# Performance work log

Measured on AMD Instinct MI355X. Metric: run time of the kernel, lower is better.

Reference implementation:

```python
import jax, jax.numpy as jnp
import numpy as np

FEATURE_DIM = 256
LN_EPS = 1e-5        # torch nn.LayerNorm default
WHITEN_EPS = 1e-4    # whitening_eps init arg


def setup_inputs() -> dict:
    key = jax.random.key(0)
    k1, _ = jax.random.split(key)
    B, T, D = 64, 2048, FEATURE_DIM
    x = jax.random.normal(k1, (B, T, D), dtype=jnp.float32)
    gamma = jnp.ones((D,), dtype=jnp.float32)
    beta = jnp.zeros((D,), dtype=jnp.float32)
    return {"x": x, "gamma": gamma, "beta": beta}


def reference(x, gamma, beta):
    # x: (B, T, D)
    B, T, D = x.shape
    # LayerNorm over last dim
    mean = jnp.mean(x, axis=-1, keepdims=True)
    var = jnp.mean((x - mean) ** 2, axis=-1, keepdims=True)
    xn = (x - mean) * jax.lax.rsqrt(var + LN_EPS) * gamma + beta
    # Batched cross-frame covariance whitening (T >= 2 here)
    mu = jnp.mean(xn, axis=1, keepdims=True)          # (B, 1, D)
    xc = xn - mu                                       # (B, T, D)
    cov = jnp.einsum('btd,bte->bde', xc, xc) / (T - 1) # (B, D, D)
    cov = cov + WHITEN_EPS * jnp.eye(D, dtype=x.dtype)
    eigvals, eigvecs = jnp.linalg.eigh(cov)            # (B, D), (B, D, D)
    inv_sqrt_vals = jax.lax.rsqrt(jnp.clip(eigvals, WHITEN_EPS, None))  # (B, D)
    # inv_sqrt = V diag(w^-1/2) V^T
    inv_sqrt = jnp.einsum('bde,be,bfe->bdf', eigvecs, inv_sqrt_vals, eigvecs)
    out = jnp.einsum('btd,bdf->btf', xc, inv_sqrt)
    return out
```

## Files before the change

kernel.cpp:

```cpp
#include <hip/hip_runtime.h>
#include <cstddef>

#define TT 2048
#define BB 64
#define DD 256
#define LN_EPS 1e-5f
#define WEPS 1e-4f

typedef __attribute__((ext_vector_type(8))) short short8;
typedef __attribute__((ext_vector_type(4))) float f32x4;
typedef __attribute__((ext_vector_type(8))) _Float16 f16x8;
typedef __attribute__((ext_vector_type(4))) _Float16 f16x4;

__device__ __forceinline__ unsigned short f2h(float f) {
  _Float16 h = (_Float16)f;
  return *(unsigned short*)&h;
}
__device__ __forceinline__ float h2f(unsigned short u) {
  _Float16 h = *(_Float16*)&u;
  return (float)h;
}
__device__ __forceinline__ void gload16(unsigned short* lds, const unsigned short* g) {
  __builtin_amdgcn_global_load_lds(
      (const __attribute__((address_space(1))) void*)g,
      (__attribute__((address_space(3))) void*)lds, 16, 0, 0);
}

__global__ __launch_bounds__(256) void prepass_kernel(const float* __restrict__ x,
    const float* __restrict__ gamma, const float* __restrict__ beta,
    unsigned short* __restrict__ A, float* __restrict__ part) {
  int c = blockIdx.x;
  int b = blockIdx.y;
  int tid = threadIdx.x;
  int wave = tid >> 6, lane = tid & 63;
  int rowbase = b * TT + c * 128 + wave * 32;
  const float* xb = x + (size_t)rowbase * DD + lane * 4;
  unsigned short* Ab = A + (size_t)rowbase * DD + lane * 4;
  float4 g4 = *(const float4*)&gamma[lane * 4];
  float4 b4 = *(const float4*)&beta[lane * 4];
  float a0 = 0.f, a1 = 0.f, a2 = 0.f, a3 = 0.f;
  for (int i = 0; i < 32; ++i) {
    float4 v = *(const float4*)&xb[(size_t)i * DD];
    float s  = v.x + v.y + v.z + v.w;
    float sq = v.x*v.x + v.y*v.y + v.z*v.z + v.w*v.w;
    #pragma unroll
    for (int off = 32; off; off >>= 1) { s += __shfl_xor(s, off); sq += __shfl_xor(sq, off); }
    float mean = s * (1.f/DD);
    float var  = fmaxf(sq * (1.f/DD) - mean*mean, 0.f);
    float rstd = rsqrtf(var + LN_EPS);
    float c0 = (v.x - mean) * rstd, c1 = (v.y - mean) * rstd;
    float c2 = (v.z - mean) * rstd, c3 = (v.w - mean) * rstd;
    a0 += c0; a1 += c1; a2 += c2; a3 += c3;
    ushort4 w;
    w.x = f2h(c0 * g4.x + b4.x);
    w.y = f2h(c1 * g4.y + b4.y);
    w.z = f2h(c2 * g4.z + b4.z);
    w.w = f2h(c3 * g4.w + b4.w);
    *(ushort4*)&Ab[(size_t)i * DD] = w;
  }
  int pidx = c * 4 + wave;
  *(float4*)&part[((size_t)pidx*BB + b)*DD + lane*4] = make_float4(a0, a1, a2, a3);
}

__global__ __launch_bounds__(256) void mu_finalize_kernel(const float* __restrict__ part,
                                                          const float* __restrict__ gamma,
                                                          const float* __restrict__ beta,
                                                          float* __restrict__ mu) {
  int b = blockIdx.x;
  int d = threadIdx.x;
  float s = 0.f;
  #pragma unroll 8
  for (int c = 0; c < 64; ++c) s += part[((size_t)c*BB + b)*DD + d];
  mu[b*DD + d] = gamma[d] * s * (1.f/TT) + beta[d];
}

__global__ __launch_bounds__(256) void cov_mfma(const unsigned short* __restrict__ A,
    const float* __restrict__ mu, unsigned short* __restrict__ Ch) {
  int flat = blockIdx.y * gridDim.x + blockIdx.x;
  int kx = flat & 7, j = flat >> 3;
  int b = (kx << 3) + j / 10;
  int tile = j - (j / 10) * 10;
  int p = 0, t = tile;
  while (t >= 4 - p) { t -= (4 - p); ++p; }
  int q = p + t;
  int i0 = p * 64, j0 = q * 64;
  bool diag = (p == q);

  __shared__ unsigned short sm[16384];
  __shared__ float sMu[128];

  int tid = threadIdx.x;
  const float* mub = mu + (size_t)b*DD;
  if (tid < 64) { sMu[tid] = mub[i0+tid]; sMu[64+tid] = mub[j0+tid]; }
  __syncthreads();

  int wave = tid >> 6, lane = tid & 63;
  int lr = lane & 15, lg = lane >> 4;
  int tg4 = tid >> 4;
  int dg  = tid & 15;
  int d0 = dg * 4;
  const unsigned short* Ab = A + (size_t)b*TT*DD;

  int ch16 = tg4 >> 1, half = tg4 & 1;
  int widx[4];
  #pragma unroll
  for (int jj = 0; jj < 4; ++jj) {
    int dl = d0 + jj;
    int swz = (ch16 ^ (dl & 7) ^ ((dl >> 3) & 7)) & 7;
    widx[jj] = dl*64 + swz*8 + half*4;
  }

  f32x4 acc[4] = {};

  #define COV_STAGE(k0v, dst)                                                  \
  {                                                                            \
    int trow = (k0v) + tg4 * 4;                                                \
    ushort4 sv0 = *(const ushort4*)&Ab[(size_t)(trow+0)*DD + i0 + d0];         \
    ushort4 sv1 = *(const ushort4*)&Ab[(size_t)(trow+1)*DD + i0 + d0];         \
    ushort4 sv2 = *(const ushort4*)&Ab[(size_t)(trow+2)*DD + i0 + d0];         \
    ushort4 sv3 = *(const ushort4*)&Ab[(size_t)(trow+3)*DD + i0 + d0];         \
    { ushort4 w = {sv0.x, sv1.x, sv2.x, sv3.x}; *(ushort4*)&(dst)[widx[0]] = w; } \
    { ushort4 w = {sv0.y, sv1.y, sv2.y, sv3.y}; *(ushort4*)&(dst)[widx[1]] = w; } \
    { ushort4 w = {sv0.z, sv1.z, sv2.z, sv3.z}; *(ushort4*)&(dst)[widx[2]] = w; } \
    { ushort4 w = {sv0.w, sv1.w, sv2.w, sv3.w}; *(ushort4*)&(dst)[widx[3]] = w; } \
    if (!diag) {                                                               \
      ushort4 t0v = *(const ushort4*)&Ab[(size_t)(trow+0)*DD + j0 + d0];       \
      ushort4 t1v = *(const ushort4*)&Ab[(size_t)(trow+1)*DD + j0 + d0];       \
      ushort4 t2v = *(const ushort4*)&Ab[(size_t)(trow+2)*DD + j0 + d0];       \
      ushort4 t3v = *(const ushort4*)&Ab[(size_t)(trow+3)*DD + j0 + d0];       \
      { ushort4 w = {t0v.x, t1v.x, t2v.x, t3v.x}; *(ushort4*)&(dst)[4096 + widx[0]] = w; } \
      { ushort4 w = {t0v.y, t1v.y, t2v.y, t3v.y}; *(ushort4*)&(dst)[4096 + widx[1]] = w; } \
      { ushort4 w = {t0v.z, t1v.z, t2v.z, t3v.z}; *(ushort4*)&(dst)[4096 + widx[2]] = w; } \
      { ushort4 w = {t0v.w, t1v.w, t2v.w, t3v.w}; *(ushort4*)&(dst)[4096 + widx[3]] = w; } \
    }                                                                          \
  }

  COV_STAGE(0, sm);
  __syncthreads();

  for (int kk = 0; kk < 32; ++kk) {
    unsigned short* cur = sm + (kk & 1) * 8192;
    if (kk < 31) {
      unsigned short* nxt = sm + ((kk & 1) ^ 1) * 8192;
      COV_STAGE((kk + 1) * 64, nxt);
    }
    const unsigned short* pA = cur;
    const unsigned short* pB = diag ? cur : (cur + 4096);
    #pragma unroll
    for (int ks = 0; ks < 2; ++ks) {
      int rowA = wave*16 + lr;
      int cc = ks*4 + lg;
      int aoff = rowA*64 + (((cc ^ (rowA&7) ^ ((rowA>>3)&7)) & 7) << 3);
      f16x8 av = *(const f16x8*)&pA[aoff];
      #pragma unroll
      for (int n = 0; n < 4; ++n) {
        int rowB = n*16 + lr;
        int boff = rowB*64 + (((cc ^ (rowB&7) ^ ((rowB>>3)&7)) & 7) << 3);
        f16x8 bv = *(const f16x8*)&pB[boff];
        acc[n] = __builtin_amdgcn_mfma_f32_16x16x32_f16(av, bv, acc[n], 0, 0, 0);
      }
    }
    __syncthreads();
  }
  #undef COV_STAGE

  float* sC = (float*)sm;
  #pragma unroll
  for (int n = 0; n < 4; ++n)
    #pragma unroll
    for (int r = 0; r < 4; ++r)
      sC[(wave*16 + lg*4 + r)*65 + n*16 + lr] = acc[n][r];
  __syncthreads();
  unsigned short* Chb = Ch + (size_t)b*DD*DD;
  const float invTm1 = 1.f / (float)(TT - 1);
  int row = tid >> 2, cb = (tid & 3) * 16;
  int gi = i0 + row;
  float mi = sMu[row] * (float)TT;
  unsigned short hv[16];
  #pragma unroll
  for (int e = 0; e < 16; ++e) {
    int gj = j0 + cb + e;
    float v = (sC[row*65 + cb + e] - mi * sMu[64 + cb + e]) * invTm1;
    if (gi == gj) v += WEPS;
    hv[e] = f2h(v);
    if (!diag) Chb[(size_t)gj*DD + gi] = hv[e];
  }
  size_t go = (size_t)gi*DD + j0 + cb;
  *(short8*)&Chb[go]     = *(short8*)&hv[0];
  *(short8*)&Chb[go + 8] = *(short8*)&hv[8];
}

__global__ __launch_bounds__(256) void power_kernel(
    const unsigned short* __restrict__ Ch, float* __restrict__ sbuf) {
  int b = blockIdx.x, tid = threadIdx.x;
  __shared__ unsigned short sC[DD*DD];
  __shared__ float v[DD];
  __shared__ float red[4];
  const unsigned short* Cb = Ch + (size_t)b*DD*DD;
  #pragma unroll
  for (int i = 0; i < 32; ++i) {
    int chunkid = i*256 + tid;
    int r = chunkid >> 5, ch = chunkid & 31;
    short8 qv = *(const short8*)&Cb[(size_t)chunkid*8];
    *(short8*)&sC[r*256 + ((ch ^ (r & 7)) << 3)] = qv;
  }
  unsigned u = (unsigned)tid * 2654435761u;
  v[tid] = 0.5f + (float)((u >> 9) & 1023) * (1.f/1024.f);
  __syncthreads();
  float lam = 1.f;
  for (int it = 0; it < 10; ++it) {
    float w = 0.f;
    #pragma unroll
    for (int ch = 0; ch < 32; ++ch) {
      short8 hq = *(const short8*)&sC[tid*256 + ((ch ^ (tid & 7)) << 3)];
      const float* vp = &v[ch*8];
      #pragma unroll
      for (int e = 0; e < 8; ++e) w += h2f((unsigned short)hq[e]) * vp[e];
    }
    float ssq = w * w;
    #pragma unroll
    for (int off = 32; off; off >>= 1) ssq += __shfl_xor(ssq, off);
    if ((tid & 63) == 0) red[tid >> 6] = ssq;
    __syncthreads();
    float nrm = sqrtf(red[0] + red[1] + red[2] + red[3]);
    lam = nrm;
    v[tid] = w / nrm;
    __syncthreads();
  }
  if (tid == 0) sbuf[b] = lam * 1.05f;
}

__device__ __forceinline__ void bgemm_tile2(
    const unsigned short* __restrict__ A, const unsigned short* __restrict__ B,
    unsigned short* __restrict__ C,
    float alpha, float diagBeta, int tilex, int b, unsigned short* sm) {
  const int tid = threadIdx.x;
  const int i0g = (tilex >> 1) * 128, j0g = (tilex & 1) * 128;
  const size_t mb = (size_t)b * DD * DD;
  const int wave = tid >> 6, lane = tid & 63;
  const int wr = wave >> 2, wc = wave & 3;
  const int lr = lane & 15, lg = lane >> 4;

  f32x4 acc[8] = {};

  #pragma unroll
  for (int p2 = 0; p2 < 2; ++p2) {
    int slot = tid + p2 * 512;
    int row = slot >> 3, c = slot & 7;
    int srcc = (c ^ (row & 7)) << 3;
    int base = (wave * 64 + p2 * 512) * 8;
    gload16(&sm[base], A + mb + (size_t)(i0g + row) * DD + srcc);
    gload16(&sm[8192 + base], B + mb + (size_t)(j0g + row) * DD + srcc);
  }
  __syncthreads();

  #pragma unroll
  for (int kk = 0; kk < 4; ++kk) {
    unsigned short* cur = sm + (kk & 1) * 16384;
    if (kk < 3) {
      unsigned short* nxt = sm + ((kk & 1) ^ 1) * 16384;
      int k0n = (kk + 1) * 64;
      #pragma unroll
      for (int p2 = 0; p2 < 2; ++p2) {
        int slot = tid + p2 * 512;
        int row = slot >> 3, c = slot & 7;
        int srcc = (c ^ (row & 7)) << 3;
        int base = (wave * 64 + p2 * 512) * 8;
        gload16(&nxt[base], A + mb + (size_t)(i0g + row) * DD + k0n + srcc);
        gload16(&nxt[8192 + base], B + mb + (size_t)(j0g + row) * DD + k0n + srcc);
      }
    }
    #pragma unroll
    for (int ks = 0; ks < 2; ++ks) {
      int cc = ks * 4 + lg;
      f16x8 bv[2];
      #pragma unroll
      for (int n = 0; n < 2; ++n) {
        int rowB = wc * 32 + n * 16 + lr;
        int boff = rowB * 64 + ((cc ^ (rowB & 7)) * 8);
        bv[n] = *(const f16x8*)&cur[8192 + boff];
      }
      #pragma unroll
      for (int m = 0; m < 4; ++m) {
        int rowA = wr * 64 + m * 16 + lr;
        int aoff = rowA * 64 + ((cc ^ (rowA & 7)) * 8);
        f16x8 av = *(const f16x8*)&cur[aoff];
        #pragma unroll
        for (int n = 0; n < 2; ++n)
          acc[m*2+n] = __builtin_amdgcn_mfma_f32_16x16x32_f16(av, bv[n], acc[m*2+n], 0, 0, 0);
      }
    }
    __syncthreads();
  }

  #pragma unroll
  for (int m = 0; m < 4; ++m) {
    #pragma unroll
    for (int n = 0; n < 2; ++n) {
      int col = j0g + wc * 32 + n * 16 + lr;
      int row0 = i0g + wr * 64 + m * 16 + lg * 4;
      #pragma unroll
      for (int r = 0; r < 4; ++r) {
        float vv = alpha * acc[m*2+n][r];
        int row = row0 + r;
        if (row == col) vv += diagBeta;
        C[mb + (size_t)row * DD + col] = f2h(vv);
      }
    }
  }
}

__global__ __launch_bounds__(512) void bgemm_mfma2(
    const unsigned short* __restrict__ A, const unsigned short* __restrict__ B,
    unsigned short* __restrict__ C, float alpha, float diagBeta) {
  __shared__ unsigned short sm[32768];
  int flat = blockIdx.y * gridDim.x + blockIdx.x;
  int kx = flat & 7, j = flat >> 3;
  int b = (kx << 3) + (j >> 2);
  int tile = j & 3;
  bgemm_tile2(A, B, C, alpha, diagBeta, tile, b, sm);
}

__global__ __launch_bounds__(512) void bgemm_dual2(
    const unsigned short* __restrict__ A0, const unsigned short* __restrict__ B0,
    unsigned short* __restrict__ C0,
    const unsigned short* __restrict__ A1, const unsigned short* __restrict__ B1,
    unsigned short* __restrict__ C1) {
  __shared__ unsigned short sm[32768];
  int flat = blockIdx.y * gridDim.x + blockIdx.x;
  int kx = flat & 7, j = flat >> 3;
  int b = (kx << 3) + (j >> 3);
  int t8 = j & 7;
  int half = t8 >> 2, tile = t8 & 3;
  if (half == 0)
    bgemm_tile2(A0, B0, C0, 0.5f, 0.f, tile, b, sm);
  else
    bgemm_tile2(A1, B1, C1, 0.5f, 0.f, tile, b, sm);
}

__global__ __launch_bounds__(512) void bgemm_p0(
    const unsigned short* __restrict__ C, unsigned short* __restrict__ Y1,
    unsigned short* __restrict__ Z1, const float* __restrict__ sbuf) {
  __shared__ unsigned short sm[32768];
  int flat = blockIdx.y * gridDim.x + blockIdx.x;
  int kx = flat & 7, j = flat >> 3;
  int b = (kx << 3) + (j >> 2);
  int tilex = j & 3;

  const int tid = threadIdx.x;
  const int i0g = (tilex >> 1) * 128, j0g = (tilex & 1) * 128;
  const size_t mb = (size_t)b * DD * DD;
  const int wave = tid >> 6, lane = tid & 63;
  const int wr = wave >> 2, wc = wave & 3;
  const int lr = lane & 15, lg = lane >> 4;

  f32x4 acc[8] = {};

  #pragma unroll
  for (int p2 = 0; p2 < 2; ++p2) {
    int slot = tid + p2 * 512;
    int row = slot >> 3, c = slot & 7;
    int srcc = (c ^ (row & 7)) << 3;
    int base = (wave * 64 + p2 * 512) * 8;
    gload16(&sm[base], C + mb + (size_t)(i0g + row) * DD + srcc);
    gload16(&sm[8192 + base], C + mb + (size_t)(j0g + row) * DD + srcc);
  }
  __syncthreads();

  #pragma unroll
  for (int kk = 0; kk < 4; ++kk) {
    unsigned short* cur = sm + (kk & 1) * 16384;
    if (kk < 3) {
      unsigned short* nxt = sm + ((kk & 1) ^ 1) * 16384;
      int k0n = (kk + 1) * 64;
      #pragma unroll
      for (int p2 = 0; p2 < 2; ++p2) {
        int slot = tid + p2 * 512;
        int row = slot >> 3, c = slot & 7;
        int srcc = (c ^ (row & 7)) << 3;
        int base = (wave * 64 + p2 * 512) * 8;
        gload16(&nxt[base], C + mb + (size_t)(i0g + row) * DD + k0n + srcc);
        gload16(&nxt[8192 + base], C + mb + (size_t)(j0g + row) * DD + k0n + srcc);
      }
    }
    #pragma unroll
    for (int ks = 0; ks < 2; ++ks) {
      int cc = ks * 4 + lg;
      f16x8 bv[2];
      #pragma unroll
      for (int n = 0; n < 2; ++n) {
        int rowB = wc * 32 + n * 16 + lr;
        int boff = rowB * 64 + ((cc ^ (rowB & 7)) * 8);
        bv[n] = *(const f16x8*)&cur[8192 + boff];
      }
      #pragma unroll
      for (int m = 0; m < 4; ++m) {
        int rowA = wr * 64 + m * 16 + lr;
        int aoff = rowA * 64 + ((cc ^ (rowA & 7)) * 8);
        f16x8 av = *(const f16x8*)&cur[aoff];
        #pragma unroll
        for (int n = 0; n < 2; ++n)
          acc[m*2+n] = __builtin_amdgcn_mfma_f32_16x16x32_f16(av, bv[n], acc[m*2+n], 0, 0, 0);
      }
    }
    __syncthreads();
  }

  float invs = 1.f / sbuf[b];
  float a2 = -invs * invs;
  float a1c = 2.f * invs;
  float z1c = -invs;
  #pragma unroll
  for (int m = 0; m < 4; ++m) {
    #pragma unroll
    for (int n = 0; n < 2; ++n) {
      int col = j0g + wc * 32 + n * 16 + lr;
      int row0 = i0g + wr * 64 + m * 16 + lg * 4;
      #pragma unroll
      for (int r = 0; r < 4; ++r) {
        int row = row0 + r;
        float cv = h2f(C[mb + (size_t)row * DD + col]);
        float yv = a2 * acc[m*2+n][r] + a1c * cv;
        float zv = z1c * cv + ((row == col) ? 2.f : 0.f);
        Y1[mb + (size_t)row * DD + col] = f2h(yv);
        Z1[mb + (size_t)row * DD + col] = f2h(zv);
      }
    }
  }
}

__global__ __launch_bounds__(256) void matvec_r(const float* __restrict__ mu,
    const unsigned short* __restrict__ W, float* __restrict__ rvec) {
  int b = blockIdx.x, f = threadIdx.x;
  __shared__ float sMu[DD];
  sMu[f] = mu[(size_t)b*DD + f];
  __syncthreads();
  const unsigned short* Wb = W + (size_t)b*DD*DD;
  float acc = 0.f;
  #pragma unroll 8
  for (int d = 0; d < DD; ++d) acc += sMu[d] * h2f(Wb[(size_t)d*DD + f]);
  rvec[(size_t)b*DD + f] = acc;
}

__global__ __launch_bounds__(512) void out_mfma2(const unsigned short* __restrict__ A,
    const unsigned short* __restrict__ W, const float* __restrict__ rvec,
    const float* __restrict__ sbuf, float* __restrict__ out) {
  int flat = blockIdx.y * gridDim.x + blockIdx.x;
  int kx = flat & 7, j = flat >> 3;
  int b = (kx << 3) + (j >> 5);
  int tile = j & 31;
  int t0 = (tile >> 1) * 128, f0 = (tile & 1) * 128;
  __shared__ unsigned short sm[32768];

  int tid = threadIdx.x;
  const int wave = tid >> 6, lane = tid & 63;
  const int wr = wave >> 2, wc = wave & 3;
  const int lr = lane & 15, lg = lane >> 4;
  const unsigned short* Ab = A + (size_t)b*TT*DD;
  const unsigned short* Wb = W + (size_t)b*DD*DD;

  f32x4 acc[8] = {};

  #pragma unroll
  for (int p2 = 0; p2 < 2; ++p2) {
    int slot = tid + p2 * 512;
    int row = slot >> 3, c = slot & 7;
    int srcc = (c ^ (row & 7)) << 3;
    int base = (wave * 64 + p2 * 512) * 8;
    gload16(&sm[base], Ab + (size_t)(t0 + row) * DD + srcc);
    gload16(&sm[8192 + base], Wb + (size_t)(f0 + row) * DD + srcc);
  }
  __syncthreads();

  #pragma unroll
  for (int kk = 0; kk < 4; ++kk) {
    unsigned short* cur = sm + (kk & 1) * 16384;
    if (kk < 3) {
      unsigned short* nxt = sm + ((kk & 1) ^ 1) * 16384;
      int k0n = (kk + 1) * 64;
      #pragma unroll
      for (int p2 = 0; p2 < 2; ++p2) {
        int slot = tid + p2 * 512;
        int row = slot >> 3, c = slot & 7;
        int srcc = (c ^ (row & 7)) << 3;
        int base = (wave * 64 + p2 * 512) * 8;
        gload16(&nxt[base], Ab + (size_t)(t0 + row) * DD + k0n + srcc);
        gload16(&nxt[8192 + base], Wb + (size_t)(f0 + row) * DD + k0n + srcc);
      }
    }
    #pragma unroll
    for (int ks = 0; ks < 2; ++ks) {
      int cc = ks * 4 + lg;
      f16x8 bv[2];
      #pragma unroll
      for (int n = 0; n < 2; ++n) {
        int rowB = wc * 32 + n * 16 + lr;
        int boff = rowB * 64 + ((cc ^ (rowB & 7)) * 8);
        bv[n] = *(const f16x8*)&cur[8192 + boff];
      }
      #pragma unroll
      for (int m = 0; m < 4; ++m) {
        int rowA = wr * 64 + m * 16 + lr;
        int aoff = rowA * 64 + ((cc ^ (rowA & 7)) * 8);
        f16x8 av = *(const f16x8*)&cur[aoff];
        #pragma unroll
        for (int n = 0; n < 2; ++n)
          acc[m*2+n] = __builtin_amdgcn_mfma_f32_16x16x32_f16(av, bv[n], acc[m*2+n], 0, 0, 0);
      }
    }
    __syncthreads();
  }

  float rs = rsqrtf(sbuf[b]);
  float rv[2];
  #pragma unroll
  for (int n = 0; n < 2; ++n)
    rv[n] = rvec[(size_t)b*DD + f0 + wc*32 + n*16 + lr];
  float* ob = out + (size_t)b*TT*DD;
  #pragma unroll
  for (int m = 0; m < 4; ++m) {
    #pragma unroll
    for (int n = 0; n < 2; ++n) {
      int col = f0 + wc * 32 + n * 16 + lr;
      int row0 = t0 + wr * 64 + m * 16 + lg * 4;
      #pragma unroll
      for (int r = 0; r < 4; ++r)
        ob[(size_t)(row0 + r)*DD + col] = (acc[m*2+n][r] - rv[n]) * rs;
    }
  }
}

extern "C" void kernel_launch(void* const* d_in, const int* in_sizes, int n_in,
                              void* d_out, int out_size, void* d_ws, size_t ws_size,
                              hipStream_t stream) {
  const float* x     = (const float*)d_in[0];
  const float* gamma = (const float*)d_in[1];
  const float* beta  = (const float*)d_in[2];
  float* out = (float*)d_out;

  float* wsf  = (float*)d_ws;
  float* mu   = wsf;
  float* sbuf = wsf + 16384;
  float* rvec = wsf + 16448;
  unsigned short* nsb = (unsigned short*)(wsf + 32832);
  const size_t MATU = (size_t)BB * DD * DD;
  unsigned short* H[5];
  for (int k = 0; k < 5; ++k) H[k] = nsb + (size_t)k * MATU;
  unsigned short* A = nsb + 5 * MATU;
  float* part = (float*)H[1];

  prepass_kernel<<<dim3(16, BB), 256, 0, stream>>>(x, gamma, beta, A, part);
  mu_finalize_kernel<<<BB, 256, 0, stream>>>(part, gamma, beta, mu);
  cov_mfma<<<dim3(10, BB), 256, 0, stream>>>(A, mu, H[0]);
  power_kernel<<<BB, 256, 0, stream>>>(H[0], sbuf);

  bgemm_p0<<<dim3(4, BB), 512, 0, stream>>>(H[0], H[3], H[1], sbuf);
  bgemm_mfma2<<<dim3(4, BB), 512, 0, stream>>>(H[1], H[3], H[2], -1.f, 3.f);
  bgemm_dual2<<<dim3(8, BB), 512, 0, stream>>>(H[3], H[2], H[0],
                                               H[2], H[1], H[4]);
  bgemm_mfma2<<<dim3(4, BB), 512, 0, stream>>>(H[4], H[0], H[2], -1.f, 3.f);
  bgemm_mfma2<<<dim3(4, BB), 512, 0, stream>>>(H[2], H[4], H[1], 0.5f, 0.f);

  matvec_r<<<BB, 256, 0, stream>>>(mu, H[1], rvec);
  out_mfma2<<<dim3(32, BB), 512, 0, stream>>>(A, H[1], rvec, sbuf, out);
}
```

Measured before the change: 199.8 us.

## Exploit symmetry in Newton-Schulz GEMMs, fuse mu finalize, widen power iteration

The separate mu-finalize kernel is removed. Its reduction now happens inside cov_mfma, which computes the 128 mu values it needs, and inside power_kernel, which writes mu for later kernels. Because the iterated matrices are symmetric, the bgemm kernels compute only the three upper-triangular 128x128 tiles and write the off-diagonal tile's transpose through LDS, cutting the GEMM grids from 256 to 192 blocks. power_kernel uses 512 threads with two threads per row, and output stores become nontemporal. The risk is that the mirrored writes rely on exact symmetry of products of commuting matrices; fp16 rounding may make them slightly asymmetric.

```diff
diff --git a/kernel.cpp b/kernel.cpp
--- a/kernel.cpp
+++ b/kernel.cpp
@@ -62,20 +62,9 @@
   *(float4*)&part[((size_t)pidx*BB + b)*DD + lane*4] = make_float4(a0, a1, a2, a3);
 }
 
-__global__ __launch_bounds__(256) void mu_finalize_kernel(const float* __restrict__ part,
-                                                          const float* __restrict__ gamma,
-                                                          const float* __restrict__ beta,
-                                                          float* __restrict__ mu) {
-  int b = blockIdx.x;
-  int d = threadIdx.x;
-  float s = 0.f;
-  #pragma unroll 8
-  for (int c = 0; c < 64; ++c) s += part[((size_t)c*BB + b)*DD + d];
-  mu[b*DD + d] = gamma[d] * s * (1.f/TT) + beta[d];
-}
-
 __global__ __launch_bounds__(256) void cov_mfma(const unsigned short* __restrict__ A,
-    const float* __restrict__ mu, unsigned short* __restrict__ Ch) {
+    const float* __restrict__ part, const float* __restrict__ gamma,
+    const float* __restrict__ beta, unsigned short* __restrict__ Ch) {
   int flat = blockIdx.y * gridDim.x + blockIdx.x;
   int kx = flat & 7, j = flat >> 3;
   int b = (kx << 3) + j / 10;
@@ -90,8 +79,13 @@
   __shared__ float sMu[128];
 
   int tid = threadIdx.x;
-  const float* mub = mu + (size_t)b*DD;
-  if (tid < 64) { sMu[tid] = mub[i0+tid]; sMu[64+tid] = mub[j0+tid]; }
+  if (tid < 128) {
+    int dg_ = (tid < 64) ? (i0 + tid) : (j0 + tid - 64);
+    float s = 0.f;
+    #pragma unroll 8
+    for (int c = 0; c < 64; ++c) s += part[((size_t)c*BB + b)*DD + dg_];
+    sMu[tid] = gamma[dg_] * s * (1.f/TT) + beta[dg_];
+  }
   __syncthreads();
 
   int wave = tid >> 6, lane = tid & 63;
@@ -190,41 +184,52 @@
   *(short8*)&Chb[go + 8] = *(short8*)&hv[8];
 }
 
-__global__ __launch_bounds__(256) void power_kernel(
-    const unsigned short* __restrict__ Ch, float* __restrict__ sbuf) {
+__global__ __launch_bounds__(512) void power_kernel(
+    const unsigned short* __restrict__ Ch, const float* __restrict__ part,
+    const float* __restrict__ gamma, const float* __restrict__ beta,
+    float* __restrict__ mu, float* __restrict__ sbuf) {
   int b = blockIdx.x, tid = threadIdx.x;
   __shared__ unsigned short sC[DD*DD];
   __shared__ float v[DD];
-  __shared__ float red[4];
+  __shared__ float red[8];
   const unsigned short* Cb = Ch + (size_t)b*DD*DD;
   #pragma unroll
-  for (int i = 0; i < 32; ++i) {
-    int chunkid = i*256 + tid;
+  for (int i = 0; i < 16; ++i) {
+    int chunkid = i*512 + tid;
     int r = chunkid >> 5, ch = chunkid & 31;
     short8 qv = *(const short8*)&Cb[(size_t)chunkid*8];
     *(short8*)&sC[r*256 + ((ch ^ (r & 7)) << 3)] = qv;
   }
-  unsigned u = (unsigned)tid * 2654435761u;
-  v[tid] = 0.5f + (float)((u >> 9) & 1023) * (1.f/1024.f);
-  __syncthreads();
+  if (tid < DD) {
+    unsigned u = (unsigned)tid * 2654435761u;
+    v[tid] = 0.5f + (float)((u >> 9) & 1023) * (1.f/1024.f);
+    float s = 0.f;
+    #pragma unroll 8
+    for (int c = 0; c < 64; ++c) s += part[((size_t)c*BB + b)*DD + tid];
+    mu[(size_t)b*DD + tid] = gamma[tid] * s * (1.f/TT) + beta[tid];
+  }
+  __syncthreads();
+  int row = tid >> 1, half = tid & 1;
   float lam = 1.f;
   for (int it = 0; it < 10; ++it) {
     float w = 0.f;
     #pragma unroll
-    for (int ch = 0; ch < 32; ++ch) {
-      short8 hq = *(const short8*)&sC[tid*256 + ((ch ^ (tid & 7)) << 3)];
+    for (int i = 0; i < 16; ++i) {
+      int ch = half * 16 + i;
+      short8 hq = *(const short8*)&sC[row*256 + ((ch ^ (row & 7)) << 3)];
       const float* vp = &v[ch*8];
       #pragma unroll
       for (int e = 0; e < 8; ++e) w += h2f((unsigned short)hq[e]) * vp[e];
     }
-    float ssq = w * w;
+    w += __shfl_xor(w, 1);
+    float ssq = half ? 0.f : w * w;
     #pragma unroll
     for (int off = 32; off; off >>= 1) ssq += __shfl_xor(ssq, off);
     if ((tid & 63) == 0) red[tid >> 6] = ssq;
     __syncthreads();
-    float nrm = sqrtf(red[0] + red[1] + red[2] + red[3]);
+    float nrm = sqrtf(red[0]+red[1]+red[2]+red[3]+red[4]+red[5]+red[6]+red[7]);
     lam = nrm;
-    v[tid] = w / nrm;
+    if (half == 0) v[row] = w / nrm;
     __syncthreads();
   }
   if (tid == 0) sbuf[b] = lam * 1.05f;
@@ -232,10 +237,11 @@
 
 __device__ __forceinline__ void bgemm_tile2(
     const unsigned short* __restrict__ A, const unsigned short* __restrict__ B,
-    unsigned short* __restrict__ C,
-    float alpha, float diagBeta, int tilex, int b, unsigned short* sm) {
+    unsigned short* __restrict__ Cc,
+    float alpha, float diagBeta, int ti, int tj, int b, unsigned short* sm) {
   const int tid = threadIdx.x;
-  const int i0g = (tilex >> 1) * 128, j0g = (tilex & 1) * 128;
+  const int i0g = ti * 128, j0g = tj * 128;
+  const bool mirror = (ti != tj);
   const size_t mb = (size_t)b * DD * DD;
   const int wave = tid >> 6, lane = tid & 63;
   const int wr = wave >> 2, wc = wave & 3;
@@ -293,6 +299,7 @@
     __syncthreads();
   }
 
+  unsigned short hvv[4][2][4];
   #pragma unroll
   for (int m = 0; m < 4; ++m) {
     #pragma unroll
@@ -304,9 +311,33 @@
         float vv = alpha * acc[m*2+n][r];
         int row = row0 + r;
         if (row == col) vv += diagBeta;
-        C[mb + (size_t)row * DD + col] = f2h(vv);
-      }
-    }
+        unsigned short h = f2h(vv);
+        hvv[m][n][r] = h;
+        Cc[mb + (size_t)row * DD + col] = h;
+      }
+    }
+  }
+
+  if (mirror) {
+    #pragma unroll
+    for (int m = 0; m < 4; ++m)
+      #pragma unroll
+      for (int n = 0; n < 2; ++n) {
+        int lcol = wc * 32 + n * 16 + lr;
+        int lrow0 = wr * 64 + m * 16 + lg * 4;
+        #pragma unroll
+        for (int r = 0; r < 4; ++r)
+          sm[lcol * 128 + ((lrow0 + r) ^ ((lcol & 7) << 3))] = hvv[m][n][r];
+      }
+    __syncthreads();
+    #pragma unroll
+    for (int ci = 0; ci < 4; ++ci) {
+      int chunk = tid + ci * 512;
+      int mr = chunk >> 4, mc0 = (chunk & 15) * 8;
+      f16x8 v = *(const f16x8*)&sm[mr * 128 + (mc0 ^ ((mr & 7) << 3))];
+      *(f16x8*)&Cc[mb + (size_t)(j0g + mr) * DD + i0g + mc0] = v;
+    }
+    __syncthreads();
   }
 }
 
@@ -314,11 +345,11 @@
     const unsigned short* __restrict__ A, const unsigned short* __restrict__ B,
     unsigned short* __restrict__ C, float alpha, float diagBeta) {
   __shared__ unsigned short sm[32768];
-  int flat = blockIdx.y * gridDim.x + blockIdx.x;
+  int flat = blockIdx.x;
   int kx = flat & 7, j = flat >> 3;
-  int b = (kx << 3) + (j >> 2);
-  int tile = j & 3;
-  bgemm_tile2(A, B, C, alpha, diagBeta, tile, b, sm);
+  int b = (kx << 3) + j / 3;
+  int ut = j - (j / 3) * 3;
+  bgemm_tile2(A, B, C, alpha, diagBeta, ut >> 1, (ut + 1) >> 1, b, sm);
 }
 
 __global__ __launch_bounds__(512) void bgemm_dual2(
@@ -327,28 +358,31 @@
     const unsigned short* __restrict__ A1, const unsigned short* __restrict__ B1,
     unsigned short* __restrict__ C1) {
   __shared__ unsigned short sm[32768];
-  int flat = blockIdx.y * gridDim.x + blockIdx.x;
+  int flat = blockIdx.x;
   int kx = flat & 7, j = flat >> 3;
-  int b = (kx << 3) + (j >> 3);
-  int t8 = j & 7;
-  int half = t8 >> 2, tile = t8 & 3;
+  int b = (kx << 3) + j / 6;
+  int t6 = j - (j / 6) * 6;
+  int half = t6 >= 3 ? 1 : 0;
+  int ut = t6 - half * 3;
   if (half == 0)
-    bgemm_tile2(A0, B0, C0, 0.5f, 0.f, tile, b, sm);
+    bgemm_tile2(A0, B0, C0, 0.5f, 0.f, ut >> 1, (ut + 1) >> 1, b, sm);
   else
-    bgemm_tile2(A1, B1, C1, 0.5f, 0.f, tile, b, sm);
+    bgemm_tile2(A1, B1, C1, 0.5f, 0.f, ut >> 1, (ut + 1) >> 1, b, sm);
 }
 
 __global__ __launch_bounds__(512) void bgemm_p0(
     const unsigned short* __restrict__ C, unsigned short* __restrict__ Y1,
     unsigned short* __restrict__ Z1, const float* __restrict__ sbuf) {
   __shared__ unsigned short sm[32768];
-  int flat = blockIdx.y * gridDim.x + blockIdx.x;
+  int flat = blockIdx.x;
   int kx = flat & 7, j = flat >> 3;
-  int b = (kx << 3) + (j >> 2);
-  int tilex = j & 3;
+  int b = (kx << 3) + j / 3;
+  int ut = j - (j / 3) * 3;
+  int ti = ut >> 1, tj = (ut + 1) >> 1;
+  bool mirror = (ti != tj);
 
   const int tid = threadIdx.x;
-  const int i0g = (tilex >> 1) * 128, j0g = (tilex & 1) * 128;
+  const int i0g = ti * 128, j0g = tj * 128;
   const size_t mb = (size_t)b * DD * DD;
   const int wave = tid >> 6, lane = tid & 63;
   const int wr = wave >> 2, wc = wave & 3;
@@ -410,6 +444,7 @@
   float a2 = -invs * invs;
   float a1c = 2.f * invs;
   float z1c = -invs;
+  unsigned short yvv[4][2][4], zvv[4][2][4];
   #pragma unroll
   for (int m = 0; m < 4; ++m) {
     #pragma unroll
@@ -422,9 +457,38 @@
         float cv = h2f(C[mb + (size_t)row * DD + col]);
         float yv = a2 * acc[m*2+n][r] + a1c * cv;
         float zv = z1c * cv + ((row == col) ? 2.f : 0.f);
-        Y1[mb + (size_t)row * DD + col] = f2h(yv);
-        Z1[mb + (size_t)row * DD + col] = f2h(zv);
-      }
+        unsigned short yh = f2h(yv), zh = f2h(zv);
+        yvv[m][n][r] = yh; zvv[m][n][r] = zh;
+        Y1[mb + (size_t)row * DD + col] = yh;
+        Z1[mb + (size_t)row * DD + col] = zh;
+      }
+    }
+  }
+  if (mirror) {
+    #pragma unroll
+    for (int m = 0; m < 4; ++m)
+      #pragma unroll
+      for (int n = 0; n < 2; ++n) {
+        int lcol = wc * 32 + n * 16 + lr;
+        int lrow0 = wr * 64 + m * 16 + lg * 4;
+        #pragma unroll
+        for (int r = 0; r < 4; ++r) {
+          int idx = lcol * 128 + ((lrow0 + r) ^ ((lcol & 7) << 3));
+          sm[idx] = yvv[m][n][r];
+          sm[16384 + idx] = zvv[m][n][r];
+        }
+      }
+    __syncthreads();
+    #pragma unroll
+    for (int ci = 0; ci < 4; ++ci) {
+      int chunk = tid + ci * 512;
+      int mr = chunk >> 4, mc0 = (chunk & 15) * 8;
+      int idx = mr * 128 + (mc0 ^ ((mr & 7) << 3));
+      f16x8 vy = *(const f16x8*)&sm[idx];
+      f16x8 vz = *(const f16x8*)&sm[16384 + idx];
+      size_t go = mb + (size_t)(j0g + mr) * DD + i0g + mc0;
+      *(f16x8*)&Y1[go] = vy;
+      *(f16x8*)&Z1[go] = vz;
     }
   }
 }
@@ -525,7 +589,8 @@
       int row0 = t0 + wr * 64 + m * 16 + lg * 4;
       #pragma unroll
       for (int r = 0; r < 4; ++r)
-        ob[(size_t)(row0 + r)*DD + col] = (acc[m*2+n][r] - rv[n]) * rs;
+        __builtin_nontemporal_store((acc[m*2+n][r] - rv[n]) * rs,
+                                    &ob[(size_t)(row0 + r)*DD + col]);
     }
   }
 }
@@ -547,19 +612,18 @@
   unsigned short* H[5];
   for (int k = 0; k < 5; ++k) H[k] = nsb + (size_t)k * MATU;
   unsigned short* A = nsb + 5 * MATU;
-  float* part = (float*)H[1];
+  float* part = (float*)H[3];
 
   prepass_kernel<<<dim3(16, BB), 256, 0, stream>>>(x, gamma, beta, A, part);
-  mu_finalize_kernel<<<BB, 256, 0, stream>>>(part, gamma, beta, mu);
-  cov_mfma<<<dim3(10, BB), 256, 0, stream>>>(A, mu, H[0]);
-  power_kernel<<<BB, 256, 0, stream>>>(H[0], sbuf);
-
-  bgemm_p0<<<dim3(4, BB), 512, 0, stream>>>(H[0], H[3], H[1], sbuf);
-  bgemm_mfma2<<<dim3(4, BB), 512, 0, stream>>>(H[1], H[3], H[2], -1.f, 3.f);
-  bgemm_dual2<<<dim3(8, BB), 512, 0, stream>>>(H[3], H[2], H[0],
-                                               H[2], H[1], H[4]);
-  bgemm_mfma2<<<dim3(4, BB), 512, 0, stream>>>(H[4], H[0], H[2], -1.f, 3.f);
-  bgemm_mfma2<<<dim3(4, BB), 512, 0, stream>>>(H[2], H[4], H[1], 0.5f, 0.f);
+  cov_mfma<<<dim3(10, BB), 256, 0, stream>>>(A, part, gamma, beta, H[0]);
+  power_kernel<<<BB, 512, 0, stream>>>(H[0], part, gamma, beta, mu, sbuf);
+
+  bgemm_p0<<<dim3(192), 512, 0, stream>>>(H[0], H[3], H[1], sbuf);
+  bgemm_mfma2<<<dim3(192), 512, 0, stream>>>(H[1], H[3], H[2], -1.f, 3.f);
+  bgemm_dual2<<<dim3(384), 512, 0, stream>>>(H[3], H[2], H[0],
+                                             H[2], H[1], H[4]);
+  bgemm_mfma2<<<dim3(192), 512, 0, stream>>>(H[4], H[0], H[2], -1.f, 3.f);
+  bgemm_mfma2<<<dim3(192), 512, 0, stream>>>(H[2], H[4], H[1], 0.5f, 0.f);
 
   matvec_r<<<BB, 256, 0, stream>>>(mu, H[1], rvec);
   out_mfma2<<<dim3(32, BB), 512, 0, stream>>>(A, H[1], rvec, sbuf, out);
```

Result: no change. 198.0 us (-0.9%).
